# Kernel tuning notes

Hardware: AMD Instinct MI355X
Metric: run time of the kernel (lower is better)

Reference implementation:

```python
import jax, jax.numpy as jnp
import numpy as np

D_MODEL = 768
N_HEADS = 12
D_HEAD = D_MODEL // N_HEADS
B, T = 2, 4096


def setup_inputs() -> dict:
    key = jax.random.key(0)
    ks = jax.random.split(key, 9)
    s = 1.0 / np.sqrt(D_MODEL)
    x = jax.random.normal(ks[0], (B, T, D_MODEL), dtype=jnp.float32)
    Wq = jax.random.uniform(ks[1], (D_MODEL, D_MODEL), jnp.float32, -s, s)
    Wk = jax.random.uniform(ks[2], (D_MODEL, D_MODEL), jnp.float32, -s, s)
    Wv = jax.random.uniform(ks[3], (D_MODEL, D_MODEL), jnp.float32, -s, s)
    Wo = jax.random.uniform(ks[4], (D_MODEL, D_MODEL), jnp.float32, -s, s)
    bq = jax.random.uniform(ks[5], (D_MODEL,), jnp.float32, -s, s)
    bk = jax.random.uniform(ks[6], (D_MODEL,), jnp.float32, -s, s)
    bv = jax.random.uniform(ks[7], (D_MODEL,), jnp.float32, -s, s)
    bo = jax.random.uniform(ks[8], (D_MODEL,), jnp.float32, -s, s)
    return {"x": x, "Wq": Wq, "bq": bq, "Wk": Wk, "bk": bk,
            "Wv": Wv, "bv": bv, "Wo": Wo, "bo": bo}


def _split_heads(t):
    # [B, T, D] -> [B, H, T, d_head]
    Bc, Tc, _ = t.shape
    return t.reshape(Bc, Tc, N_HEADS, D_HEAD).transpose(0, 2, 1, 3)


def reference(x, Wq, bq, Wk, bk, Wv, bv, Wo, bo):
    scale = D_HEAD ** -0.5
    Q = _split_heads(x @ Wq.T + bq)
    K = _split_heads(x @ Wk.T + bk)
    V = _split_heads(x @ Wv.T + bv)
    scores = jnp.einsum('bhqd,bhkd->bhqk', Q, K) * scale  # [B,H,T,T]
    attn = jax.nn.softmax(scores, axis=-1)
    out = jnp.einsum('bhqk,bhkd->bhqd', attn, V)  # [B,H,T,d_head]
    out = out.transpose(0, 2, 1, 3).reshape(x.shape[0], x.shape[1], D_MODEL)
    return out @ Wo.T + bo
```

## Files before the change

### kernel.cpp

```cpp
#include <hip/hip_runtime.h>
#include <hip/hip_bf16.h>

#define DM 768
#define NH 12
#define TB 2
#define TT 4096
#define MM (TB*TT)
#define NQKV (3*DM)
#define NW (DM*DM)
#define NX (MM*DM)
#define CEQ 0.18033688f

typedef unsigned short u16;
typedef short s16x8 __attribute__((ext_vector_type(8)));
typedef unsigned short u16x8 __attribute__((ext_vector_type(8)));
typedef float f32x4 __attribute__((ext_vector_type(4)));
typedef float f32x16 __attribute__((ext_vector_type(16)));
typedef unsigned u32x4 __attribute__((ext_vector_type(4)));

#if __has_builtin(__builtin_amdgcn_exp2f)
#define EXP2 __builtin_amdgcn_exp2f
#else
#define EXP2 exp2f
#endif

__device__ __forceinline__ u16 f2bf(float f) {
  unsigned u = __builtin_bit_cast(unsigned, f);
  unsigned r = (u + 0x7FFFu + ((u >> 16) & 1u)) >> 16;
  return (u16)r;
}

__device__ __forceinline__ unsigned cvtpk(float lo, float hi) {
  unsigned r;
  asm("v_cvt_pk_bf16_f32 %0, %1, %2" : "=v"(r) : "v"(lo), "v"(hi));
  return r;
}

__device__ __forceinline__ void gload16(const void* g, void* l) {
  __builtin_amdgcn_global_load_lds(
      (const __attribute__((address_space(1))) void*)g,
      (__attribute__((address_space(3))) void*)l, 16, 0, 0);
}

__device__ __forceinline__ void plswap(unsigned a, unsigned b, unsigned& r0, unsigned& r1) {
#if __has_builtin(__builtin_amdgcn_permlane32_swap)
  auto rr = __builtin_amdgcn_permlane32_swap(a, b, false, false);
  unsigned tmp[2];
  __builtin_memcpy(tmp, &rr, 8);
  r0 = tmp[0]; r1 = tmp[1];
#else
  int hi_ = (threadIdx.x >> 5) & 1;
  unsigned bx = (unsigned)__shfl_xor((int)b, 32, 64);
  unsigned ax = (unsigned)__shfl_xor((int)a, 32, 64);
  r0 = hi_ ? bx : a;
  r1 = hi_ ? b : ax;
#endif
}

__device__ __forceinline__ float xhalf_sum(float v) {
  unsigned a = __builtin_bit_cast(unsigned, v), r0, r1;
  plswap(a, a, r0, r1);
  return __builtin_bit_cast(float, r0) + __builtin_bit_cast(float, r1);
}

__device__ __forceinline__ void repack2(const f32x16& sv, s16x8& fa, s16x8& fb) {
  {
    unsigned cA0 = cvtpk(sv[0], sv[1]),  cA1 = cvtpk(sv[2], sv[3]);
    unsigned cB0 = cvtpk(sv[4], sv[5]),  cB1 = cvtpk(sv[6], sv[7]);
    unsigned w0, w1, w2, w3;
    plswap(cA0, cB0, w0, w2);
    plswap(cA1, cB1, w1, w3);
    u32x4 w = {w0, w1, w2, w3};
    fa = __builtin_bit_cast(s16x8, w);
  }
  {
    unsigned cA0 = cvtpk(sv[8], sv[9]),   cA1 = cvtpk(sv[10], sv[11]);
    unsigned cB0 = cvtpk(sv[12], sv[13]), cB1 = cvtpk(sv[14], sv[15]);
    unsigned w0, w1, w2, w3;
    plswap(cA0, cB0, w0, w2);
    plswap(cA1, cB1, w1, w3);
    u32x4 w = {w0, w1, w2, w3};
    fb = __builtin_bit_cast(s16x8, w);
  }
}

__global__ __launch_bounds__(256) void cast_prep(
    const float* __restrict__ x, const float* __restrict__ wq,
    const float* __restrict__ wk, const float* __restrict__ wv,
    const float* __restrict__ wo, const float* __restrict__ bq,
    const float* __restrict__ bk, const float* __restrict__ bv,
    u16* __restrict__ xb, u16* __restrict__ wqkvb, u16* __restrict__ wob,
    float* __restrict__ bqkv) {
  int g = blockIdx.x * 256 + threadIdx.x;
  int e = g * 4;
  const float* src;
  u16* dst;
  if (e < NX) { src = x + e; dst = xb + e; }
  else {
    int e2 = e - NX;
    if (e2 < 3*NW) {
      const float* w = (e2 < NW) ? wq : (e2 < 2*NW ? wk : wv);
      int base = (e2 < NW) ? 0 : (e2 < 2*NW ? NW : 2*NW);
      src = w + (e2 - base); dst = wqkvb + e2;
    } else { int e3 = e2 - 3*NW; src = wo + e3; dst = wob + e3; }
  }
  float4 v = *(const float4*)src;
  ushort4 p;
  p.x = f2bf(v.x); p.y = f2bf(v.y); p.z = f2bf(v.z); p.w = f2bf(v.w);
  *(ushort4*)dst = p;
  if (blockIdx.x == 0) {
    for (int i = threadIdx.x; i < NQKV; i += 256)
      bqkv[i] = (i < DM) ? bq[i] : (i < 2*DM ? bk[i-DM] : bv[i-2*DM]);
  }
}

__global__ __launch_bounds__(256, 3) void gemm_qkv(
    const u16* __restrict__ A, const u16* __restrict__ W,
    const float* __restrict__ bias,
    u16* __restrict__ qb, u16* __restrict__ kb, u16* __restrict__ vt) {
  __shared__ __align__(16) u16 As[2][128*32], Bs[2][128*32];
  const int tid = threadIdx.x, lane = tid & 63, wave = tid >> 6;
  const int rg = lane & 15, cg = lane >> 4;
  int lin = blockIdx.y * 18 + blockIdx.x;
  int swz = (lin & 7) * 144 + (lin >> 3);
  const int m0 = (swz / 18) * 128, n0 = (swz % 18) * 128;
  const int wm = (wave >> 1) * 64, wn = (wave & 1) * 64;
  f32x4 acc[4][4];
#pragma unroll
  for (int i = 0; i < 4; i++)
#pragma unroll
    for (int j = 0; j < 4; j++) acc[i][j] = (f32x4){0.f,0.f,0.f,0.f};

  const u16* ga = A + (size_t)(m0 + (tid >> 2)) * DM + (tid & 3) * 8;
  const u16* gb = W + (size_t)(n0 + (tid >> 2)) * DM + (tid & 3) * 8;
  auto stage = [&](int kt, int buf) {
    int ko = kt * 32;
    char* la = (char*)&As[buf][0] + wave * 1024;
    char* lb = (char*)&Bs[buf][0] + wave * 1024;
    gload16(ga + ko,                    la);
    gload16(ga + (size_t)64*DM + ko,    la + 4096);
    gload16(gb + ko,                    lb);
    gload16(gb + (size_t)64*DM + ko,    lb + 4096);
  };

  stage(0, 0);
  __syncthreads();
  const int NT = DM / 32;
  int cur = 0;
  for (int kt = 0; kt < NT; ++kt) {
    if (kt + 1 < NT) stage(kt + 1, cur ^ 1);
    s16x8 af[4], bfv[4];
#pragma unroll
    for (int i = 0; i < 4; i++) af[i]  = *(const s16x8*)&As[cur][(wm + i*16 + rg)*32 + cg*8];
#pragma unroll
    for (int i = 0; i < 4; i++) bfv[i] = *(const s16x8*)&Bs[cur][(wn + i*16 + rg)*32 + cg*8];
    __builtin_amdgcn_s_setprio(1);
#pragma unroll
    for (int mi = 0; mi < 4; mi++)
#pragma unroll
      for (int ni = 0; ni < 4; ni++)
        acc[mi][ni] = __builtin_amdgcn_mfma_f32_16x16x32_bf16(af[mi], bfv[ni], acc[mi][ni], 0, 0, 0);
    __builtin_amdgcn_s_setprio(0);
    __syncthreads();
    cur ^= 1;
  }

#pragma unroll
  for (int ni = 0; ni < 4; ni++) {
    int o = n0 + wn + ni*16 + rg;
    float bia = bias[o];
    int mat = o / DM, d = o % DM;
    int head = d >> 6, dh = d & 63;
    if (mat == 2) {
#pragma unroll
      for (int mi = 0; mi < 4; mi++) {
        int m = m0 + wm + mi*16 + cg*4;
        int b = m >> 12, t = m & 4095;
        ushort4 pv;
        pv.x = f2bf(acc[mi][ni][0] + bia);
        pv.y = f2bf(acc[mi][ni][1] + bia);
        pv.z = f2bf(acc[mi][ni][2] + bia);
        pv.w = f2bf(acc[mi][ni][3] + bia);
        *(ushort4*)&vt[((size_t)((b*NH + head)*64 + dh))*TT + t] = pv;
      }
    } else {
      u16* outp = mat ? kb : qb;
      float sc = mat ? 1.0f : CEQ;
#pragma unroll
      for (int mi = 0; mi < 4; mi++) {
#pragma unroll
        for (int r = 0; r < 4; r++) {
          int m = m0 + wm + mi*16 + cg*4 + r;
          int b = m >> 12, t = m & 4095;
          outp[((size_t)((b*NH + head)*TT + t))*64 + dh] = f2bf((acc[mi][ni][r] + bia) * sc);
        }
      }
    }
  }
}

__global__ __launch_bounds__(256, 3) void attn4(
    const u16* __restrict__ qg, const u16* __restrict__ kg,
    const u16* __restrict__ vtg, u16* __restrict__ h) {
  __shared__ __align__(16) char smem[32768];
  const int tid = threadIdx.x, lane = tid & 63, wave = tid >> 6;
  const int ql = lane & 31, hi = lane >> 5;
  int lin = blockIdx.y * 32 + blockIdx.x;
  int swz = (lin & 7) * 96 + (lin >> 3);
  int qt = swz & 31, bh = swz >> 5;
  const int b = bh / NH, head = bh % NH;
  const size_t hb = (size_t)bh * TT * 64;

  const int qrow = qt * 128 + wave * 32 + ql;
  const u16* qp = qg + hb + (size_t)qrow * 64 + hi * 8;
  s16x8 qf[4];
#pragma unroll
  for (int ds = 0; ds < 4; ++ds) qf[ds] = *(const s16x8*)(qp + ds * 16);

  const int lr = lane >> 3;
  const int lc = ((lane & 7) ^ lr) * 16;
  const char* kSrc = (const char*)(kg + hb) + lr * 128 + lc;
  const char* vSrc = (const char*)(vtg + hb) + (size_t)lr * 8192 + lc;
  char* ldsK = smem + wave * 2048;
  auto stage = [&](int kt, int buf) {
    char* lk = ldsK + buf * 16384;
    char* lv = lk + 8192;
    const char* gk = kSrc + (size_t)kt * 8192 + wave * 2048;
    const char* gv = vSrc + (size_t)kt * 128 + (size_t)wave * 131072;
    gload16(gk,          lk);
    gload16(gk + 1024,   lk + 1024);
    gload16(gv,          lv);
    gload16(gv + 65536,  lv + 1024);
  };

  f32x16 o0 = {}, o1 = {};
  float L = 0.f;
  const int swb = (ql & 7) << 4;

  stage(0, 0);
  __syncthreads();

  const int NKT = TT / 64;
  int cur = 0;
  for (int kt = 0; kt < NKT; ++kt) {
    if (kt + 1 < NKT) stage(kt + 1, cur ^ 1);

    const char* bk_ = smem + cur * 16384 + ql * 128;
    const char* bv_ = bk_ + 8192;

    s16x8 kf0[4], kf1[4];
#pragma unroll
    for (int ds = 0; ds < 4; ++ds) {
      kf0[ds] = *(const s16x8*)(bk_ +        ((ds*32 + hi*16) ^ swb));
      kf1[ds] = *(const s16x8*)(bk_ + 4096 + ((ds*32 + hi*16) ^ swb));
    }
    f32x16 s0 = {}, s1 = {};
    __builtin_amdgcn_s_setprio(1);
#pragma unroll
    for (int ds = 0; ds < 4; ++ds) {
      s0 = __builtin_amdgcn_mfma_f32_32x32x16_bf16(kf0[ds], qf[ds], s0, 0, 0, 0);
      s1 = __builtin_amdgcn_mfma_f32_32x32x16_bf16(kf1[ds], qf[ds], s1, 0, 0, 0);
    }
    __builtin_amdgcn_s_setprio(0);

    s16x8 vf0[4], vf1[4];
#pragma unroll
    for (int ks = 0; ks < 4; ++ks) {
      vf0[ks] = *(const s16x8*)(bv_ +        ((ks*32 + hi*16) ^ swb));
      vf1[ks] = *(const s16x8*)(bv_ + 4096 + ((ks*32 + hi*16) ^ swb));
    }

#pragma unroll
    for (int i = 0; i < 16; ++i) s0[i] = EXP2(s0[i]);
#pragma unroll
    for (int i = 0; i < 16; ++i) s1[i] = EXP2(s1[i]);
    f32x16 u = s0 + s1;
    float a0 = u[0] + u[8],  a1 = u[1] + u[9],  a2 = u[2] + u[10], a3 = u[3] + u[11];
    float a4 = u[4] + u[12], a5 = u[5] + u[13], a6 = u[6] + u[14], a7 = u[7] + u[15];
    a0 += a4; a1 += a5; a2 += a6; a3 += a7;
    a0 += a2; a1 += a3;
    L += a0 + a1;

    s16x8 pf[4];
    repack2(s0, pf[0], pf[1]);
    repack2(s1, pf[2], pf[3]);

    __builtin_amdgcn_s_setprio(1);
#pragma unroll
    for (int ks = 0; ks < 4; ++ks) {
      o0 = __builtin_amdgcn_mfma_f32_32x32x16_bf16(vf0[ks], pf[ks], o0, 0, 0, 0);
      o1 = __builtin_amdgcn_mfma_f32_32x32x16_bf16(vf1[ks], pf[ks], o1, 0, 0, 0);
    }
    __builtin_amdgcn_s_setprio(0);

    __syncthreads();
    cur ^= 1;
  }

  float Lt = xhalf_sum(L);
  float inv = 1.f / Lt;
  u16 (*ot)[32][72] = (u16(*)[32][72])smem;
#pragma unroll
  for (int db = 0; db < 2; ++db) {
    const f32x16& ov = db ? o1 : o0;
#pragma unroll
    for (int i = 0; i < 8; ++i) {
      unsigned w = cvtpk(ov[2*i] * inv, ov[2*i+1] * inv);
      int d = db*32 + ((2*i) & 3) + 8*((2*i) >> 2) + 4*hi;
      *(unsigned*)&ot[wave][ql][d] = w;
    }
  }
  __syncthreads();
  const u16* rowp = &ot[wave][ql][hi*32];
  u32x4 r0 = *(const u32x4*)(rowp);
  u32x4 r1 = *(const u32x4*)(rowp + 8);
  u32x4 r2 = *(const u32x4*)(rowp + 16);
  u32x4 r3 = *(const u32x4*)(rowp + 24);
  u16* dst = h + (size_t)(b*TT + qrow) * DM + head*64 + hi*32;
  *(u32x4*)(dst)      = r0;
  *(u32x4*)(dst + 8)  = r1;
  *(u32x4*)(dst + 16) = r2;
  *(u32x4*)(dst + 24) = r3;
}

__global__ __launch_bounds__(256, 3) void gemm_proj(
    const u16* __restrict__ A, const u16* __restrict__ W,
    const float* __restrict__ bias, float* __restrict__ out) {
  __shared__ __align__(16) u16 As[2][128*32], Bs[2][128*32];
  const int tid = threadIdx.x, lane = tid & 63, wave = tid >> 6;
  const int rg = lane & 15, cg = lane >> 4;
  int lin = blockIdx.y * 6 + blockIdx.x;
  int swz = (lin & 7) * 48 + (lin >> 3);
  const int m0 = (swz / 6) * 128, n0 = (swz % 6) * 128;
  const int wm = (wave >> 1) * 64, wn = (wave & 1) * 64;
  f32x4 acc[4][4];
#pragma unroll
  for (int i = 0; i < 4; i++)
#pragma unroll
    for (int j = 0; j < 4; j++) acc[i][j] = (f32x4){0.f,0.f,0.f,0.f};

  const u16* ga = A + (size_t)(m0 + (tid >> 2)) * DM + (tid & 3) * 8;
  const u16* gb = W + (size_t)(n0 + (tid >> 2)) * DM + (tid & 3) * 8;
  auto stage = [&](int kt, int buf) {
    int ko = kt * 32;
    char* la = (char*)&As[buf][0] + wave * 1024;
    char* lb = (char*)&Bs[buf][0] + wave * 1024;
    gload16(ga + ko,                    la);
    gload16(ga + (size_t)64*DM + ko,    la + 4096);
    gload16(gb + ko,                    lb);
    gload16(gb + (size_t)64*DM + ko,    lb + 4096);
  };

  stage(0, 0);
  __syncthreads();
  const int NT = DM / 32;
  int cur = 0;
  for (int kt = 0; kt < NT; ++kt) {
    if (kt + 1 < NT) stage(kt + 1, cur ^ 1);
    s16x8 af[4], bfv[4];
#pragma unroll
    for (int i = 0; i < 4; i++) af[i]  = *(const s16x8*)&As[cur][(wm + i*16 + rg)*32 + cg*8];
#pragma unroll
    for (int i = 0; i < 4; i++) bfv[i] = *(const s16x8*)&Bs[cur][(wn + i*16 + rg)*32 + cg*8];
    __builtin_amdgcn_s_setprio(1);
#pragma unroll
    for (int mi = 0; mi < 4; mi++)
#pragma unroll
      for (int ni = 0; ni < 4; ni++)
        acc[mi][ni] = __builtin_amdgcn_mfma_f32_16x16x32_bf16(af[mi], bfv[ni], acc[mi][ni], 0, 0, 0);
    __builtin_amdgcn_s_setprio(0);
    __syncthreads();
    cur ^= 1;
  }
#pragma unroll
  for (int ni = 0; ni < 4; ni++) {
    int o = n0 + wn + ni*16 + rg;
    float bia = bias[o];
#pragma unroll
    for (int mi = 0; mi < 4; mi++) {
#pragma unroll
      for (int r = 0; r < 4; r++) {
        int m = m0 + wm + mi*16 + cg*4 + r;
        out[(size_t)m * DM + o] = acc[mi][ni][r] + bia;
      }
    }
  }
}

extern "C" void kernel_launch(void* const* d_in, const int* in_sizes, int n_in,
                              void* d_out, int out_size, void* d_ws, size_t ws_size,
                              hipStream_t stream) {
  (void)in_sizes; (void)n_in; (void)out_size; (void)ws_size;
  const float* x  = (const float*)d_in[0];
  const float* Wq = (const float*)d_in[1];
  const float* bq = (const float*)d_in[2];
  const float* Wk = (const float*)d_in[3];
  const float* bk = (const float*)d_in[4];
  const float* Wv = (const float*)d_in[5];
  const float* bv = (const float*)d_in[6];
  const float* Wo = (const float*)d_in[7];
  const float* bo = (const float*)d_in[8];
  float* out = (float*)d_out;

  char* ws = (char*)d_ws;
  size_t off = 0;
  auto alloc = [&](size_t bytes) {
    char* p = ws + off;
    off = (off + bytes + 255) & ~(size_t)255;
    return p;
  };
  u16*   xb    = (u16*)alloc((size_t)NX * 2);
  u16*   wqkvb = (u16*)alloc((size_t)3 * NW * 2);
  u16*   wob   = (u16*)alloc((size_t)NW * 2);
  float* bqkv  = (float*)alloc((size_t)NQKV * 4);
  u16*   qb    = (u16*)alloc((size_t)NX * 2);
  u16*   kb    = (u16*)alloc((size_t)NX * 2);
  u16*   vtb   = (u16*)alloc((size_t)NX * 2);
  u16*   hbuf  = xb;

  cast_prep<<<(NX + 4*NW) / 4 / 256, 256, 0, stream>>>(x, Wq, Wk, Wv, Wo, bq, bk, bv,
                                                       xb, wqkvb, wob, bqkv);
  gemm_qkv<<<dim3(18, 64), 256, 0, stream>>>(xb, wqkvb, bqkv, qb, kb, vtb);
  attn4<<<dim3(32, TB*NH), 256, 0, stream>>>(qb, kb, vtb, hbuf);
  gemm_proj<<<dim3(6, 64), 256, 0, stream>>>(hbuf, wob, bo, out);
}
```

Before: 194.6 us.

## Give each attention wave two query tiles to reuse K/V fragments

The attention kernel now runs 2 waves per block instead of 4, and each wave handles 64 query rows as two 32-row sub-tiles. Every K and V fragment read from LDS feeds two MFMAs, which halves LDS read traffic per unit of compute. The K tile is processed in two 32-key chunks to bound register pressure. The cost is more accumulator and Q registers per wave, fewer waves per block, and an occupancy hint lowered to 2, which may reduce latency hiding.

Result: slower. 207.0 us (+6.4%).

```diff
diff --git a/kernel.cpp b/kernel.cpp
--- a/kernel.cpp
+++ b/kernel.cpp
@@ -82,6 +82,14 @@
     u32x4 w = {w0, w1, w2, w3};
     fb = __builtin_bit_cast(s16x8, w);
   }
+}
+
+__device__ __forceinline__ float tree16(const f32x16& u) {
+  float a0 = u[0] + u[8],  a1 = u[1] + u[9],  a2 = u[2] + u[10], a3 = u[3] + u[11];
+  float a4 = u[4] + u[12], a5 = u[5] + u[13], a6 = u[6] + u[14], a7 = u[7] + u[15];
+  a0 += a4; a1 += a5; a2 += a6; a3 += a7;
+  a0 += a2; a1 += a3;
+  return a0 + a1;
 }
 
 __global__ __launch_bounds__(256) void cast_prep(
@@ -199,7 +207,7 @@
   }
 }
 
-__global__ __launch_bounds__(256, 3) void attn4(
+__global__ __launch_bounds__(128, 2) void attn5(
     const u16* __restrict__ qg, const u16* __restrict__ kg,
     const u16* __restrict__ vtg, u16* __restrict__ h) {
   __shared__ __align__(16) char smem[32768];
@@ -211,30 +219,33 @@
   const int b = bh / NH, head = bh % NH;
   const size_t hb = (size_t)bh * TT * 64;
 
-  const int qrow = qt * 128 + wave * 32 + ql;
-  const u16* qp = qg + hb + (size_t)qrow * 64 + hi * 8;
-  s16x8 qf[4];
-#pragma unroll
-  for (int ds = 0; ds < 4; ++ds) qf[ds] = *(const s16x8*)(qp + ds * 16);
+  const int qrowA = qt * 128 + wave * 64 + ql;
+  const u16* qpA = qg + hb + (size_t)qrowA * 64 + hi * 8;
+  s16x8 qfA[4], qfB[4];
+#pragma unroll
+  for (int ds = 0; ds < 4; ++ds) {
+    qfA[ds] = *(const s16x8*)(qpA + ds * 16);
+    qfB[ds] = *(const s16x8*)(qpA + 32*64 + ds * 16);
+  }
 
   const int lr = lane >> 3;
   const int lc = ((lane & 7) ^ lr) * 16;
   const char* kSrc = (const char*)(kg + hb) + lr * 128 + lc;
   const char* vSrc = (const char*)(vtg + hb) + (size_t)lr * 8192 + lc;
-  char* ldsK = smem + wave * 2048;
   auto stage = [&](int kt, int buf) {
-    char* lk = ldsK + buf * 16384;
+    char* lk = smem + buf * 16384 + wave * 4096;
     char* lv = lk + 8192;
-    const char* gk = kSrc + (size_t)kt * 8192 + wave * 2048;
-    const char* gv = vSrc + (size_t)kt * 128 + (size_t)wave * 131072;
-    gload16(gk,          lk);
-    gload16(gk + 1024,   lk + 1024);
-    gload16(gv,          lv);
-    gload16(gv + 65536,  lv + 1024);
+    const char* gk = kSrc + (size_t)kt * 8192 + wave * 4096;
+    const char* gv = vSrc + (size_t)kt * 128 + (size_t)wave * 262144;
+#pragma unroll
+    for (int i = 0; i < 4; ++i) {
+      gload16(gk + i*1024,  lk + i*1024);
+      gload16(gv + i*65536, lv + i*1024);
+    }
   };
 
-  f32x16 o0 = {}, o1 = {};
-  float L = 0.f;
+  f32x16 oA0 = {}, oA1 = {}, oB0 = {}, oB1 = {};
+  float LA = 0.f, LB = 0.f;
   const int swb = (ql & 7) << 4;
 
   stage(0, 0);
@@ -244,83 +255,78 @@
   int cur = 0;
   for (int kt = 0; kt < NKT; ++kt) {
     if (kt + 1 < NKT) stage(kt + 1, cur ^ 1);
-
-    const char* bk_ = smem + cur * 16384 + ql * 128;
-    const char* bv_ = bk_ + 8192;
-
-    s16x8 kf0[4], kf1[4];
-#pragma unroll
-    for (int ds = 0; ds < 4; ++ds) {
-      kf0[ds] = *(const s16x8*)(bk_ +        ((ds*32 + hi*16) ^ swb));
-      kf1[ds] = *(const s16x8*)(bk_ + 4096 + ((ds*32 + hi*16) ^ swb));
+    const char* Kt = smem + cur * 16384;
+    const char* Vt = Kt + 8192;
+#pragma unroll
+    for (int c = 0; c < 2; ++c) {
+      const char* bkc = Kt + (c*32 + ql) * 128;
+      s16x8 kf[4];
+#pragma unroll
+      for (int ds = 0; ds < 4; ++ds)
+        kf[ds] = *(const s16x8*)(bkc + ((ds*32 + hi*16) ^ swb));
+      f32x16 sA = {}, sB = {};
+      __builtin_amdgcn_s_setprio(1);
+#pragma unroll
+      for (int ds = 0; ds < 4; ++ds) {
+        sA = __builtin_amdgcn_mfma_f32_32x32x16_bf16(kf[ds], qfA[ds], sA, 0, 0, 0);
+        sB = __builtin_amdgcn_mfma_f32_32x32x16_bf16(kf[ds], qfB[ds], sB, 0, 0, 0);
+      }
+      __builtin_amdgcn_s_setprio(0);
+      const char* bvc = Vt + ql * 128;
+      s16x8 vf[2][2];
+#pragma unroll
+      for (int hh = 0; hh < 2; ++hh)
+#pragma unroll
+        for (int kc = 0; kc < 2; ++kc)
+          vf[hh][kc] = *(const s16x8*)(bvc + hh*4096 + ((c*64 + kc*32 + hi*16) ^ swb));
+#pragma unroll
+      for (int i = 0; i < 16; ++i) sA[i] = EXP2(sA[i]);
+#pragma unroll
+      for (int i = 0; i < 16; ++i) sB[i] = EXP2(sB[i]);
+      LA += tree16(sA);
+      LB += tree16(sB);
+      s16x8 pfA[2], pfB[2];
+      repack2(sA, pfA[0], pfA[1]);
+      repack2(sB, pfB[0], pfB[1]);
+      __builtin_amdgcn_s_setprio(1);
+#pragma unroll
+      for (int kc = 0; kc < 2; ++kc) {
+        oA0 = __builtin_amdgcn_mfma_f32_32x32x16_bf16(vf[0][kc], pfA[kc], oA0, 0, 0, 0);
+        oB0 = __builtin_amdgcn_mfma_f32_32x32x16_bf16(vf[0][kc], pfB[kc], oB0, 0, 0, 0);
+        oA1 = __builtin_amdgcn_mfma_f32_32x32x16_bf16(vf[1][kc], pfA[kc], oA1, 0, 0, 0);
+        oB1 = __builtin_amdgcn_mfma_f32_32x32x16_bf16(vf[1][kc], pfB[kc], oB1, 0, 0, 0);
+      }
+      __builtin_amdgcn_s_setprio(0);
     }
-    f32x16 s0 = {}, s1 = {};
-    __builtin_amdgcn_s_setprio(1);
-#pragma unroll
-    for (int ds = 0; ds < 4; ++ds) {
-      s0 = __builtin_amdgcn_mfma_f32_32x32x16_bf16(kf0[ds], qf[ds], s0, 0, 0, 0);
-      s1 = __builtin_amdgcn_mfma_f32_32x32x16_bf16(kf1[ds], qf[ds], s1, 0, 0, 0);
-    }
-    __builtin_amdgcn_s_setprio(0);
-
-    s16x8 vf0[4], vf1[4];
-#pragma unroll
-    for (int ks = 0; ks < 4; ++ks) {
-      vf0[ks] = *(const s16x8*)(bv_ +        ((ks*32 + hi*16) ^ swb));
-      vf1[ks] = *(const s16x8*)(bv_ + 4096 + ((ks*32 + hi*16) ^ swb));
-    }
-
-#pragma unroll
-    for (int i = 0; i < 16; ++i) s0[i] = EXP2(s0[i]);
-#pragma unroll
-    for (int i = 0; i < 16; ++i) s1[i] = EXP2(s1[i]);
-    f32x16 u = s0 + s1;
-    float a0 = u[0] + u[8],  a1 = u[1] + u[9],  a2 = u[2] + u[10], a3 = u[3] + u[11];
-    float a4 = u[4] + u[12], a5 = u[5] + u[13], a6 = u[6] + u[14], a7 = u[7] + u[15];
-    a0 += a4; a1 += a5; a2 += a6; a3 += a7;
-    a0 += a2; a1 += a3;
-    L += a0 + a1;
-
-    s16x8 pf[4];
-    repack2(s0, pf[0], pf[1]);
-    repack2(s1, pf[2], pf[3]);
-
-    __builtin_amdgcn_s_setprio(1);
-#pragma unroll
-    for (int ks = 0; ks < 4; ++ks) {
-      o0 = __builtin_amdgcn_mfma_f32_32x32x16_bf16(vf0[ks], pf[ks], o0, 0, 0, 0);
-      o1 = __builtin_amdgcn_mfma_f32_32x32x16_bf16(vf1[ks], pf[ks], o1, 0, 0, 0);
-    }
-    __builtin_amdgcn_s_setprio(0);
-
     __syncthreads();
     cur ^= 1;
   }
 
-  float Lt = xhalf_sum(L);
-  float inv = 1.f / Lt;
-  u16 (*ot)[32][72] = (u16(*)[32][72])smem;
+  float invA = 1.f / xhalf_sum(LA);
+  float invB = 1.f / xhalf_sum(LB);
+  u16 (*ot)[72] = (u16(*)[72])smem;
 #pragma unroll
   for (int db = 0; db < 2; ++db) {
-    const f32x16& ov = db ? o1 : o0;
+    const f32x16& ovA = db ? oA1 : oA0;
+    const f32x16& ovB = db ? oB1 : oB0;
 #pragma unroll
     for (int i = 0; i < 8; ++i) {
-      unsigned w = cvtpk(ov[2*i] * inv, ov[2*i+1] * inv);
       int d = db*32 + ((2*i) & 3) + 8*((2*i) >> 2) + 4*hi;
-      *(unsigned*)&ot[wave][ql][d] = w;
+      *(unsigned*)&ot[wave*64 + ql][d]      = cvtpk(ovA[2*i]*invA, ovA[2*i+1]*invA);
+      *(unsigned*)&ot[wave*64 + 32 + ql][d] = cvtpk(ovB[2*i]*invB, ovB[2*i+1]*invB);
     }
   }
   __syncthreads();
-  const u16* rowp = &ot[wave][ql][hi*32];
-  u32x4 r0 = *(const u32x4*)(rowp);
-  u32x4 r1 = *(const u32x4*)(rowp + 8);
-  u32x4 r2 = *(const u32x4*)(rowp + 16);
-  u32x4 r3 = *(const u32x4*)(rowp + 24);
-  u16* dst = h + (size_t)(b*TT + qrow) * DM + head*64 + hi*32;
-  *(u32x4*)(dst)      = r0;
-  *(u32x4*)(dst + 8)  = r1;
-  *(u32x4*)(dst + 16) = r2;
-  *(u32x4*)(dst + 24) = r3;
+  const int row = wave*64 + lane;
+  const u16* rowp = ot[row];
+  const int qrow = qt*128 + row;
+  u16* dst = h + (size_t)(b*TT + qrow) * DM + head*64;
+#pragma unroll
+  for (int i = 0; i < 4; ++i)
+    *(u32x4*)(dst + i*16) = *(const u32x4*)(rowp + i*16);
+#pragma unroll
+  for (int i = 0; i < 4; ++i)
+    *(u32x4*)(dst + i*16 + 8) = *(const u32x4*)(rowp + i*16 + 8);
 }
 
 __global__ __launch_bounds__(256, 3) void gemm_proj(
@@ -421,6 +427,6 @@
   cast_prep<<<(NX + 4*NW) / 4 / 256, 256, 0, stream>>>(x, Wq, Wk, Wv, Wo, bq, bk, bv,
                                                        xb, wqkvb, wob, bqkv);
   gemm_qkv<<<dim3(18, 64), 256, 0, stream>>>(xb, wqkvb, bqkv, qb, kb, vtb);
-  attn4<<<dim3(32, TB*NH), 256, 0, stream>>>(qb, kb, vtb, hbuf);
+  attn5<<<dim3(32, TB*NH), 128, 0, stream>>>(qb, kb, vtb, hbuf);
   gemm_proj<<<dim3(6, 64), 256, 0, stream>>>(hbuf, wob, bo, out);
 }
```
